# Kernel tuning notes

Hardware: AMD Instinct MI355X
Metric: run time of the kernel (lower is better)

## Reference

```python
import jax, jax.numpy as jnp
import numpy as np

B, T, D, A = 32, 4096, 256, 128

def setup_inputs() -> dict:
    key = jax.random.key(0)
    k1, k2, k3, k4 = jax.random.split(key, 4)
    return {
        "h": jax.random.normal(k1, (B, T, D), dtype=jnp.float32),
        "W_w": jax.random.normal(k2, (A, D), dtype=jnp.float32),
        "b_w": jax.random.normal(k3, (A,), dtype=jnp.float32),
        "u_w": jax.random.normal(k4, (A,), dtype=jnp.float32),
    }

def reference(h, W_w, b_w, u_w):
    # u = tanh(h @ W_w^T + b_w)  -> [B, T, A]
    u = jnp.tanh(jnp.einsum("btd,ad->bta", h, W_w) + b_w)
    # score = u . u_w            -> [B, T]
    score = jnp.einsum("bta,a->bt", u, u_w)
    # softmax over sequence axis (stable form of exp/sum in original)
    alpha = jax.nn.softmax(score, axis=-1)  # [B, T]
    # weighted sum pooling over T -> [B, D]
    s = jnp.einsum("bt,btd->bd", alpha, h)
    return s
```

## Files before the change

### kernel.cpp

```cpp
#include <hip/hip_runtime.h>

#define B_ 32
#define T_ 4096
#define D_ 256
#define A_ 128

typedef __attribute__((ext_vector_type(8))) short bf16x8;
typedef __attribute__((ext_vector_type(4))) float f32x4;
typedef __attribute__((address_space(3))) void lds_void_t;
typedef const __attribute__((address_space(1))) void gbl_void_t;

__device__ __forceinline__ ushort f32_to_bf16_rne(float x) {
    uint u = __float_as_uint(x);
    u = (u + 0x7FFFu + ((u >> 16) & 1u)) >> 16;
    return (ushort)u;
}
__device__ __forceinline__ float bf16_bits_to_f32(ushort b) {
    return __uint_as_float(((uint)b) << 16);
}

__device__ __forceinline__ float fast_tanh(float x) {
    float t = __expf(2.0f * x);
    float r = __builtin_amdgcn_rcpf(t + 1.0f);
    return fmaf(-2.0f, r, 1.0f);
}

__device__ __forceinline__ void split8(float4 a, float4 b, bf16x8& hi8, bf16x8& lo8) {
    float xs[8] = {a.x, a.y, a.z, a.w, b.x, b.y, b.z, b.w};
    union { uint w[4]; bf16x8 v; } H, L;
#pragma unroll
    for (int p = 0; p < 4; ++p) {
        float x0 = xs[2 * p], x1 = xs[2 * p + 1];
        uint r0 = __float_as_uint(x0) + 0x8000u;
        uint r1 = __float_as_uint(x1) + 0x8000u;
        H.w[p] = __builtin_amdgcn_perm(r1, r0, 0x07060302u);
        float rem0 = x0 - __uint_as_float(r0 & 0xFFFF0000u);
        float rem1 = x1 - __uint_as_float(r1 & 0xFFFF0000u);
        L.w[p] = __builtin_amdgcn_perm(__float_as_uint(rem1), __float_as_uint(rem0), 0x07060302u);
    }
    hi8 = H.v;
    lo8 = L.v;
}

__global__ __launch_bounds__(256) void convert_W_kernel(
    const float* __restrict__ W, ushort* __restrict__ Wimg)
{
    const int c   = blockIdx.x * 256 + threadIdx.x;
    const int ph  = c >> 11;
    const int p   = (c >> 10) & 1;
    const int r   = (c >> 3) & 127;
    const int sp  = c & 7;
    const int s   = sp ^ (r & 7);
    const float* src = W + (size_t)r * D_ + ph * 64 + s * 8;

    union { ushort us[8]; float4 v; } out;
#pragma unroll
    for (int i = 0; i < 8; ++i) {
        float x = src[i];
        ushort hb = f32_to_bf16_rne(x);
        out.us[i] = p ? f32_to_bf16_rne(x - bf16_bits_to_f32(hb)) : hb;
    }
    *reinterpret_cast<float4*>(Wimg + (size_t)c * 8) = out.v;
}

__global__ __launch_bounds__(512, 2) void score_pool_kernel(
    const float* __restrict__ h, const ushort* __restrict__ Wimg,
    const float* __restrict__ bw, const float* __restrict__ uw,
    float* __restrict__ part, float2* __restrict__ stats)
{
    __shared__ char smem[163840];
    char* wlds = smem;
    char* ht   = smem + 131072;

    const int tid  = threadIdx.x;
    const int w    = tid >> 6;
    const int lane = tid & 63;
    const int l15  = lane & 15;
    const int l4   = lane >> 4;
    const int blk  = blockIdx.x;
    const size_t blkrow = (size_t)blk * 512;

    float bwv[8], uwv[8];
#pragma unroll
    for (int j = 0; j < 8; ++j) { bwv[j] = bw[j * 16 + l15]; uwv[j] = uw[j * 16 + l15]; }
    __builtin_amdgcn_sched_barrier(0);

    const float* hlane = h + (blkrow + (size_t)w * 16 + l15) * D_ + l4 * 4;

#define HSTAGE(s2, buf)                                                         \
    {                                                                           \
        const float* s0_ = hlane + (size_t)((s2) >> 3) * 128 * D_ + ((s2) & 7) * 32; \
        char* d_ = ht + (buf) * 16384 + w * 2048;                               \
        __builtin_amdgcn_global_load_lds((gbl_void_t*)(s0_),      (lds_void_t*)(d_),        16, 0, 0); \
        __builtin_amdgcn_global_load_lds((gbl_void_t*)(s0_ + 16), (lds_void_t*)(d_ + 1024), 16, 0, 0); \
    }

#pragma unroll
    for (int i = 0; i < 16; ++i)
        __builtin_amdgcn_global_load_lds(
            (gbl_void_t*)((const char*)Wimg + i * 8192 + tid * 16),
            (lds_void_t*)(wlds + i * 8192 + w * 1024), 16, 0, 0);
    HSTAGE(0, 0);
    HSTAGE(1, 1);
    asm volatile("s_waitcnt vmcnt(4)" ::: "memory");
    __builtin_amdgcn_sched_barrier(0);
    __builtin_amdgcn_s_barrier();
    __builtin_amdgcn_sched_barrier(0);

    const int reg0 = (l4 >> 1) * 1024;
    const int rd0  = w * 2048 + reg0 + (((l4 * 2)     & 3) * 16 + l15) * 16;
    const int rd1  = w * 2048 + reg0 + (((l4 * 2 + 1) & 3) * 16 + l15) * 16;

    f32x4 acc[8];
#pragma unroll
    for (int j = 0; j < 8; ++j)
#pragma unroll
        for (int r = 0; r < 4; ++r) acc[j][r] = 0.f;

    float4 pacc[4];
    float  m_arr[4], s_arr[4];

#pragma unroll
    for (int g = 0; g < 4; ++g) {
#pragma unroll
        for (int kk = 0; kk < 8; ++kk) {
            const int s = g * 8 + kk;
            if (s == 31) { asm volatile("s_waitcnt vmcnt(0)" ::: "memory"); }
            else         { asm volatile("s_waitcnt vmcnt(2)" ::: "memory"); }
            __builtin_amdgcn_sched_barrier(0);

            const int buf = s & 1;
            float4 x0 = *reinterpret_cast<const float4*>(ht + buf * 16384 + rd0);
            float4 x1 = *reinterpret_cast<const float4*>(ht + buf * 16384 + rd1);
            asm volatile("s_waitcnt lgkmcnt(0)" ::: "memory");
            __builtin_amdgcn_sched_barrier(0);
            if (s + 2 < 32) HSTAGE(s + 2, buf);

            bf16x8 ahi, alo;
            split8(x0, x1, ahi, alo);

            const int chunk = kk >> 1;
            const int slot  = (kk & 1) * 4 + l4;
#pragma unroll
            for (int j = 0; j < 8; ++j) {
                const int row = j * 16 + l15;
                const int off = chunk * 32768 + row * 128 + ((slot ^ (row & 7)) << 4);
                bf16x8 wh = *reinterpret_cast<const bf16x8*>(wlds + off);
                bf16x8 wl = *reinterpret_cast<const bf16x8*>(wlds + 16384 + off);
                acc[j] = __builtin_amdgcn_mfma_f32_16x16x32_bf16(ahi, wh, acc[j], 0, 0, 0);
                acc[j] = __builtin_amdgcn_mfma_f32_16x16x32_bf16(alo, wh, acc[j], 0, 0, 0);
                acc[j] = __builtin_amdgcn_mfma_f32_16x16x32_bf16(ahi, wl, acc[j], 0, 0, 0);
            }
        }

        float rsum[4] = {0.f, 0.f, 0.f, 0.f};
#pragma unroll
        for (int j = 0; j < 8; ++j)
#pragma unroll
            for (int r = 0; r < 4; ++r) {
                rsum[r] = fmaf(fast_tanh(acc[j][r] + bwv[j]), uwv[j], rsum[r]);
                acc[j][r] = 0.f;
            }
#pragma unroll
        for (int r = 0; r < 4; ++r) {
#pragma unroll
            for (int m = 1; m < 16; m <<= 1)
                rsum[r] += __shfl_xor(rsum[r], m, 64);
        }
        float sc16[16];
#pragma unroll
        for (int rr = 0; rr < 16; ++rr)
            sc16[rr] = __shfl(rsum[rr & 3], (rr >> 2) << 4, 64);

        float m_w = sc16[0];
#pragma unroll
        for (int rr = 1; rr < 16; ++rr) m_w = fmaxf(m_w, sc16[rr]);
        float e16[16], s_w = 0.f;
#pragma unroll
        for (int rr = 0; rr < 16; ++rr) { e16[rr] = __expf(sc16[rr] - m_w); s_w += e16[rr]; }

        const float* hg = h + (blkrow + (size_t)g * 128 + w * 16) * D_ + lane * 4;
        float4 pg = {0.f, 0.f, 0.f, 0.f};
#pragma unroll
        for (int r = 0; r < 16; ++r) {
            float4 v = *reinterpret_cast<const float4*>(hg + (size_t)r * D_);
            pg.x = fmaf(e16[r], v.x, pg.x);
            pg.y = fmaf(e16[r], v.y, pg.y);
            pg.z = fmaf(e16[r], v.z, pg.z);
            pg.w = fmaf(e16[r], v.w, pg.w);
        }
        pacc[g]  = pg;
        m_arr[g] = m_w;
        s_arr[g] = s_w;

        asm volatile("s_waitcnt vmcnt(0)" ::: "memory");
        __builtin_amdgcn_sched_barrier(0);
    }
#undef HSTAGE

    float2* mst = (float2*)wlds;
    float*  Pl  = (float*)ht;
    __syncthreads();
#pragma unroll
    for (int g = 0; g < 4; ++g) {
        const int cid = g * 8 + w;
        *reinterpret_cast<float4*>(Pl + cid * 256 + lane * 4) = pacc[g];
        if (lane == 0) mst[cid] = make_float2(m_arr[g], s_arr[g]);
    }
    __syncthreads();
    if (tid < 256) {
        float M = -3.0e38f;
#pragma unroll
        for (int c = 0; c < 32; ++c) M = fmaxf(M, mst[c].x);
        float wc[32], S = 0.f;
#pragma unroll
        for (int c = 0; c < 32; ++c) {
            wc[c] = __expf(mst[c].x - M);
            S = fmaf(wc[c], mst[c].y, S);
        }
        float p = 0.f;
#pragma unroll
        for (int c = 0; c < 32; ++c) p = fmaf(wc[c], Pl[c * 256 + tid], p);
        part[(size_t)blk * 256 + tid] = p;
        if (tid == 0) stats[blk] = make_float2(M, S);
    }
}

__global__ __launch_bounds__(256) void combine_kernel(
    const float* __restrict__ part, const float2* __restrict__ stats,
    float* __restrict__ out)
{
    const int b = blockIdx.x;
    const int t = threadIdx.x;

    float m8[8], s8[8];
    float Mg = -3.0e38f;
#pragma unroll
    for (int c = 0; c < 8; ++c) {
        float2 st = stats[b * 8 + c];
        m8[c] = st.x; s8[c] = st.y;
        Mg = fmaxf(Mg, st.x);
    }
    float wc[8], S = 0.f;
#pragma unroll
    for (int c = 0; c < 8; ++c) {
        wc[c] = __expf(m8[c] - Mg);
        S = fmaf(wc[c], s8[c], S);
    }
    const float invS = 1.0f / S;

    float acc = 0.f;
#pragma unroll
    for (int c = 0; c < 8; ++c)
        acc = fmaf(wc[c], part[((size_t)b * 8 + c) * D_ + t], acc);
    out[b * D_ + t] = acc * invS;
}

extern "C" void kernel_launch(void* const* d_in, const int* in_sizes, int n_in,
                              void* d_out, int out_size, void* d_ws, size_t ws_size,
                              hipStream_t stream) {
    const float* h  = (const float*)d_in[0];
    const float* W  = (const float*)d_in[1];
    const float* bw = (const float*)d_in[2];
    const float* uw = (const float*)d_in[3];
    float* out = (float*)d_out;

    ushort* Wimg  = (ushort*)d_ws;
    float*  part  = (float*)(Wimg + (size_t)65536);
    float2* stats = (float2*)(part + (size_t)256 * D_);

    convert_W_kernel<<<dim3(32), 256, 0, stream>>>(W, Wimg);
    score_pool_kernel<<<dim3(256), 512, 0, stream>>>(h, Wimg, bw, uw, part, stats);
    combine_kernel<<<dim3(B_), 256, 0, stream>>>(part, stats, out);
}
```

Before: 50.41 us.

## Stash bf16 h tile in LDS for pooling and halve resident W image

The pooling step now reads h from a bf16 copy of the hi part kept in LDS, written during the GEMM staging, instead of re-reading fp32 h from global memory. The W image in LDS is halved and reloaded per D-half, with barriers and a full vmcnt(0) wait every four steps. This removes the second global pass over h and shrinks LDS use, but adds serializing W reloads and rounds h to bf16 in the pooled sum, which costs accuracy.

```diff
diff --git a/kernel.cpp b/kernel.cpp
--- a/kernel.cpp
+++ b/kernel.cpp
@@ -70,7 +70,8 @@
 {
     __shared__ char smem[163840];
     char* wlds = smem;
-    char* ht   = smem + 131072;
+    char* ht   = smem + 65536;
+    char* hb16 = smem + 98304;
 
     const int tid  = threadIdx.x;
     const int w    = tid >> 6;
@@ -85,21 +86,26 @@
     for (int j = 0; j < 8; ++j) { bwv[j] = bw[j * 16 + l15]; uwv[j] = uw[j * 16 + l15]; }
     __builtin_amdgcn_sched_barrier(0);
 
-    const float* hlane = h + (blkrow + (size_t)w * 16 + l15) * D_ + l4 * 4;
+#define WSTAGE(hf)                                                             \
+    {                                                                          \
+        _Pragma("unroll")                                                      \
+        for (int i = 0; i < 8; ++i)                                            \
+            __builtin_amdgcn_global_load_lds(                                  \
+                (gbl_void_t*)((const char*)Wimg + (hf) * 65536 + i * 8192 + tid * 16), \
+                (lds_void_t*)(wlds + i * 8192 + w * 1024), 16, 0, 0);          \
+    }
 
 #define HSTAGE(s2, buf)                                                         \
     {                                                                           \
-        const float* s0_ = hlane + (size_t)((s2) >> 3) * 128 * D_ + ((s2) & 7) * 32; \
+        const int g_ = (s2) >> 3, hf_ = ((s2) >> 2) & 1, kk_ = (s2) & 3;        \
+        const float* s0_ = h + (blkrow + g_ * 128 + (size_t)w * 16 + l15) * D_  \
+                             + hf_ * 128 + kk_ * 32 + l4 * 4;                   \
         char* d_ = ht + (buf) * 16384 + w * 2048;                               \
         __builtin_amdgcn_global_load_lds((gbl_void_t*)(s0_),      (lds_void_t*)(d_),        16, 0, 0); \
         __builtin_amdgcn_global_load_lds((gbl_void_t*)(s0_ + 16), (lds_void_t*)(d_ + 1024), 16, 0, 0); \
     }
 
-#pragma unroll
-    for (int i = 0; i < 16; ++i)
-        __builtin_amdgcn_global_load_lds(
-            (gbl_void_t*)((const char*)Wimg + i * 8192 + tid * 16),
-            (lds_void_t*)(wlds + i * 8192 + w * 1024), 16, 0, 0);
+    WSTAGE(0);
     HSTAGE(0, 0);
     HSTAGE(1, 1);
     asm volatile("s_waitcnt vmcnt(4)" ::: "memory");
@@ -121,85 +127,104 @@
     float  m_arr[4], s_arr[4];
 
 #pragma unroll
-    for (int g = 0; g < 4; ++g) {
-#pragma unroll
-        for (int kk = 0; kk < 8; ++kk) {
-            const int s = g * 8 + kk;
-            if (s == 31) { asm volatile("s_waitcnt vmcnt(0)" ::: "memory"); }
-            else         { asm volatile("s_waitcnt vmcnt(2)" ::: "memory"); }
-            __builtin_amdgcn_sched_barrier(0);
-
-            const int buf = s & 1;
-            float4 x0 = *reinterpret_cast<const float4*>(ht + buf * 16384 + rd0);
-            float4 x1 = *reinterpret_cast<const float4*>(ht + buf * 16384 + rd1);
+    for (int s = 0; s < 32; ++s) {
+        const int g   = s >> 3;
+        const int hf  = (s >> 2) & 1;
+        const int kkl = s & 3;
+        const int buf = s & 1;
+
+        if ((s & 3) == 0 && s > 0) {
             asm volatile("s_waitcnt lgkmcnt(0)" ::: "memory");
             __builtin_amdgcn_sched_barrier(0);
-            if (s + 2 < 32) HSTAGE(s + 2, buf);
-
-            bf16x8 ahi, alo;
-            split8(x0, x1, ahi, alo);
-
-            const int chunk = kk >> 1;
-            const int slot  = (kk & 1) * 4 + l4;
-#pragma unroll
-            for (int j = 0; j < 8; ++j) {
-                const int row = j * 16 + l15;
-                const int off = chunk * 32768 + row * 128 + ((slot ^ (row & 7)) << 4);
-                bf16x8 wh = *reinterpret_cast<const bf16x8*>(wlds + off);
-                bf16x8 wl = *reinterpret_cast<const bf16x8*>(wlds + 16384 + off);
-                acc[j] = __builtin_amdgcn_mfma_f32_16x16x32_bf16(ahi, wh, acc[j], 0, 0, 0);
-                acc[j] = __builtin_amdgcn_mfma_f32_16x16x32_bf16(alo, wh, acc[j], 0, 0, 0);
-                acc[j] = __builtin_amdgcn_mfma_f32_16x16x32_bf16(ahi, wl, acc[j], 0, 0, 0);
+            __builtin_amdgcn_s_barrier();
+            __builtin_amdgcn_sched_barrier(0);
+            WSTAGE(hf);
+            asm volatile("s_waitcnt vmcnt(0)" ::: "memory");
+            __builtin_amdgcn_sched_barrier(0);
+            __builtin_amdgcn_s_barrier();
+            __builtin_amdgcn_sched_barrier(0);
+        } else if (s == 31) {
+            asm volatile("s_waitcnt vmcnt(0)" ::: "memory");
+        } else {
+            asm volatile("s_waitcnt vmcnt(2)" ::: "memory");
+        }
+        __builtin_amdgcn_sched_barrier(0);
+
+        float4 x0 = *reinterpret_cast<const float4*>(ht + buf * 16384 + rd0);
+        float4 x1 = *reinterpret_cast<const float4*>(ht + buf * 16384 + rd1);
+        asm volatile("s_waitcnt lgkmcnt(0)" ::: "memory");
+        __builtin_amdgcn_sched_barrier(0);
+        if (s + 2 < 32) HSTAGE(s + 2, buf);
+
+        bf16x8 ahi, alo;
+        split8(x0, x1, ahi, alo);
+
+        const int hslot = hf * 16 + kkl * 4 + l4;
+        *reinterpret_cast<bf16x8*>(
+            hb16 + w * 8192 + l15 * 512 + ((hslot ^ (l15 & 7)) << 4)) = ahi;
+
+        const int chunk = kkl >> 1;
+        const int slot  = (kkl & 1) * 4 + l4;
+#pragma unroll
+        for (int j = 0; j < 8; ++j) {
+            const int row = j * 16 + l15;
+            const int off = chunk * 32768 + row * 128 + ((slot ^ (row & 7)) << 4);
+            bf16x8 wh = *reinterpret_cast<const bf16x8*>(wlds + off);
+            bf16x8 wl = *reinterpret_cast<const bf16x8*>(wlds + 16384 + off);
+            acc[j] = __builtin_amdgcn_mfma_f32_16x16x32_bf16(ahi, wh, acc[j], 0, 0, 0);
+            acc[j] = __builtin_amdgcn_mfma_f32_16x16x32_bf16(alo, wh, acc[j], 0, 0, 0);
+            acc[j] = __builtin_amdgcn_mfma_f32_16x16x32_bf16(ahi, wl, acc[j], 0, 0, 0);
+        }
+
+        if ((s & 7) == 7) {
+            float rsum[4] = {0.f, 0.f, 0.f, 0.f};
+#pragma unroll
+            for (int j = 0; j < 8; ++j)
+#pragma unroll
+                for (int r = 0; r < 4; ++r) {
+                    rsum[r] = fmaf(fast_tanh(acc[j][r] + bwv[j]), uwv[j], rsum[r]);
+                    acc[j][r] = 0.f;
+                }
+#pragma unroll
+            for (int r = 0; r < 4; ++r) {
+#pragma unroll
+                for (int m = 1; m < 16; m <<= 1)
+                    rsum[r] += __shfl_xor(rsum[r], m, 64);
             }
+            float sc16[16];
+#pragma unroll
+            for (int rr = 0; rr < 16; ++rr)
+                sc16[rr] = __shfl(rsum[rr & 3], (rr >> 2) << 4, 64);
+
+            float m_w = sc16[0];
+#pragma unroll
+            for (int rr = 1; rr < 16; ++rr) m_w = fmaxf(m_w, sc16[rr]);
+            float e16[16], s_w = 0.f;
+#pragma unroll
+            for (int rr = 0; rr < 16; ++rr) { e16[rr] = __expf(sc16[rr] - m_w); s_w += e16[rr]; }
+
+            const int rslot = lane >> 1;
+            const int sub   = (lane & 1) * 8;
+            float4 pg = {0.f, 0.f, 0.f, 0.f};
+#pragma unroll
+            for (int r = 0; r < 16; ++r) {
+                const ushort4 hv = *reinterpret_cast<const ushort4*>(
+                    hb16 + w * 8192 + r * 512 + ((rslot ^ (r & 7)) << 4) + sub);
+                pg.x = fmaf(e16[r], bf16_bits_to_f32(hv.x), pg.x);
+                pg.y = fmaf(e16[r], bf16_bits_to_f32(hv.y), pg.y);
+                pg.z = fmaf(e16[r], bf16_bits_to_f32(hv.z), pg.z);
+                pg.w = fmaf(e16[r], bf16_bits_to_f32(hv.w), pg.w);
+            }
+            pacc[g]  = pg;
+            m_arr[g] = m_w;
+            s_arr[g] = s_w;
         }
-
-        float rsum[4] = {0.f, 0.f, 0.f, 0.f};
-#pragma unroll
-        for (int j = 0; j < 8; ++j)
-#pragma unroll
-            for (int r = 0; r < 4; ++r) {
-                rsum[r] = fmaf(fast_tanh(acc[j][r] + bwv[j]), uwv[j], rsum[r]);
-                acc[j][r] = 0.f;
-            }
-#pragma unroll
-        for (int r = 0; r < 4; ++r) {
-#pragma unroll
-            for (int m = 1; m < 16; m <<= 1)
-                rsum[r] += __shfl_xor(rsum[r], m, 64);
-        }
-        float sc16[16];
-#pragma unroll
-        for (int rr = 0; rr < 16; ++rr)
-            sc16[rr] = __shfl(rsum[rr & 3], (rr >> 2) << 4, 64);
-
-        float m_w = sc16[0];
-#pragma unroll
-        for (int rr = 1; rr < 16; ++rr) m_w = fmaxf(m_w, sc16[rr]);
-        float e16[16], s_w = 0.f;
-#pragma unroll
-        for (int rr = 0; rr < 16; ++rr) { e16[rr] = __expf(sc16[rr] - m_w); s_w += e16[rr]; }
-
-        const float* hg = h + (blkrow + (size_t)g * 128 + w * 16) * D_ + lane * 4;
-        float4 pg = {0.f, 0.f, 0.f, 0.f};
-#pragma unroll
-        for (int r = 0; r < 16; ++r) {
-            float4 v = *reinterpret_cast<const float4*>(hg + (size_t)r * D_);
-            pg.x = fmaf(e16[r], v.x, pg.x);
-            pg.y = fmaf(e16[r], v.y, pg.y);
-            pg.z = fmaf(e16[r], v.z, pg.z);
-            pg.w = fmaf(e16[r], v.w, pg.w);
-        }
-        pacc[g]  = pg;
-        m_arr[g] = m_w;
-        s_arr[g] = s_w;
-
-        asm volatile("s_waitcnt vmcnt(0)" ::: "memory");
-        __builtin_amdgcn_sched_barrier(0);
     }
 #undef HSTAGE
-
-    float2* mst = (float2*)wlds;
-    float*  Pl  = (float*)ht;
+#undef WSTAGE
+
+    float*  Pl  = (float*)smem;
+    float2* mst = (float2*)(smem + 32768);
     __syncthreads();
 #pragma unroll
     for (int g = 0; g < 4; ++g) {
```

Result: slower. 55.56 us (+10.2%).
